# Performance work log

Hardware: AMD Instinct MI355X
Metric: run time of the kernel (lower is better)

## Reference

```python
import jax, jax.numpy as jnp
import numpy as np

N, T, U, V = 8, 200, 50, 500
BLANK = 0
EPS = 1e-10


def setup_inputs() -> dict:
    key = jax.random.key(0)
    k1, k2, k3, k4, k5 = jax.random.split(key, 5)
    logits = jax.random.normal(k1, (N, T, U, V), jnp.float32)
    teacher_logits = jax.random.normal(k2, (N, T, U, V), jnp.float32)
    y = jax.random.randint(k3, (N, U), 1, V)            # padded labels (blank=0 used as pad)
    x_lens = jax.random.randint(k4, (N,), T // 2, T + 1)  # valid encoder frames
    y_lens = jax.random.randint(k5, (N,), U // 2, U + 1)  # valid label lengths
    return {"logits": logits, "teacher_logits": teacher_logits, "y": y,
            "x_lens": x_lens, "y_lens": y_lens}


def reference(logits, teacher_logits, y, x_lens, y_lens):
    # Efficient RNNT-KD: collapse V-dim softmax into 3 classes (label, blank, rest).
    n, t, u, v = logits.shape
    s = jax.nn.softmax(logits, axis=-1)             # (N,T,U,V)
    te = jax.nn.softmax(teacher_logits, axis=-1)    # (N,T,U,V)

    idx = jnp.broadcast_to(y[:, None, :, None], (n, t, u, 1))  # label index per (n,t,u)
    py = jnp.take_along_axis(s, idx, axis=-1)       # (N,T,U,1)
    t_py = jnp.take_along_axis(te, idx, axis=-1)
    blank = s[..., BLANK:BLANK + 1]
    t_blank = te[..., BLANK:BLANK + 1]

    rem = 1.0 - py - blank
    t_rem = 1.0 - t_py - t_blank
    t_rem = jnp.where(t_rem < 0, EPS, t_rem)        # floor negative remainders (in-place set in torch)

    student = jnp.log(jnp.clip(jnp.concatenate([py, blank, rem], axis=-1), EPS, 1.0))  # (N,T,U,3)
    teacher = jnp.concatenate([t_py, t_blank, t_rem], axis=-1)                          # (N,T,U,3)

    t_mask = (jnp.arange(t)[None, :] < x_lens[:, None]).astype(student.dtype)[:, :, None, None]
    u_mask = (jnp.arange(u)[None, :] < y_lens[:, None]).astype(student.dtype)[:, None, :, None]
    m = t_mask * u_mask
    return jnp.stack([student * m, teacher * m])    # (2,N,T,U,3)
```

## Files before the change

kernel.cpp:

```cpp
#include <hip/hip_runtime.h>

#define N_ 8
#define T_ 200
#define U_ 50
#define V_ 500
#define NTU (N_ * T_ * U_)
#define EPSF 1e-10f

#define ROWS 16
#define ROWF (ROWS * V_)
#define FULLC 31

__global__ __launch_bounds__(256) void tkd_kernel(
    const float* __restrict__ lg,
    const float* __restrict__ tl,
    const int* __restrict__ y,
    const int* __restrict__ xlen,
    const int* __restrict__ ylen,
    float* __restrict__ out)
{
    __shared__ float bufA[ROWF];
    __shared__ float bufB[ROWF];

    const int tid  = threadIdx.x;
    const int wv   = tid >> 6;
    const int ln   = tid & 63;
    const int row0 = blockIdx.x * ROWS;

    const float* gA = lg + (size_t)row0 * V_;
    const float* gB = tl + (size_t)row0 * V_;

#pragma unroll
    for (int c = wv; c < FULLC; c += 4) {
        __builtin_amdgcn_global_load_lds(
            (const __attribute__((address_space(1))) void*)(gA + c * 256 + ln * 4),
            (__attribute__((address_space(3))) void*)(&bufA[c * 256 + ln * 4]),
            16, 0, 0);
    }
    if (wv == 3) {
        __builtin_amdgcn_global_load_lds(
            (const __attribute__((address_space(1))) void*)(gA + 7936 + ln),
            (__attribute__((address_space(3))) void*)(&bufA[7936 + ln]),
            4, 0, 0);
    }
#pragma unroll
    for (int c = wv; c < FULLC; c += 4) {
        __builtin_amdgcn_global_load_lds(
            (const __attribute__((address_space(1))) void*)(gB + c * 256 + ln * 4),
            (__attribute__((address_space(3))) void*)(&bufB[c * 256 + ln * 4]),
            16, 0, 0);
    }
    if (wv == 3) {
        __builtin_amdgcn_global_load_lds(
            (const __attribute__((address_space(1))) void*)(gB + 7936 + ln),
            (__attribute__((address_space(3))) void*)(&bufB[7936 + ln]),
            4, 0, 0);
    }

    const int g   = tid >> 4;
    const int l   = tid & 15;
    const int row = row0 + g;
    const int n   = row / (T_ * U_);
    const int r2  = row - n * (T_ * U_);
    const int t   = r2 / U_;
    const int u   = r2 - t * U_;
    const int yv  = y[n * U_ + u];
    const int xl  = xlen[n];
    const int yl  = ylen[n];

    asm volatile("s_waitcnt vmcnt(8)" ::: "memory");
    __builtin_amdgcn_s_barrier();
    asm volatile("" ::: "memory");

    const float* ra = &bufA[g * V_];
    const int   ltail = (l <= 12) ? l : 12;
    const float wmask = (l <= 12) ? 1.0f : 0.0f;
    float sA = 0.f;
#pragma unroll
    for (int j = 0; j < 7; ++j) {
        const float4 v = *reinterpret_cast<const float4*>(ra + (j * 16 + l) * 4);
        sA += __expf(v.x) + __expf(v.y) + __expf(v.z) + __expf(v.w);
    }
    {
        const float4 v = *reinterpret_cast<const float4*>(ra + (112 + ltail) * 4);
        sA += wmask * (__expf(v.x) + __expf(v.y) + __expf(v.z) + __expf(v.w));
    }
#pragma unroll
    for (int off = 1; off < 16; off <<= 1) sA += __shfl_xor(sA, off, 64);
    const float ay = ra[yv];
    const float a0 = ra[0];

    asm volatile("s_waitcnt vmcnt(0)" ::: "memory");
    __builtin_amdgcn_s_barrier();
    asm volatile("" ::: "memory");

    const float* rb = &bufB[g * V_];
    float sB = 0.f;
#pragma unroll
    for (int j = 0; j < 7; ++j) {
        const float4 v = *reinterpret_cast<const float4*>(rb + (j * 16 + l) * 4);
        sB += __expf(v.x) + __expf(v.y) + __expf(v.z) + __expf(v.w);
    }
    {
        const float4 v = *reinterpret_cast<const float4*>(rb + (112 + ltail) * 4);
        sB += wmask * (__expf(v.x) + __expf(v.y) + __expf(v.z) + __expf(v.w));
    }
#pragma unroll
    for (int off = 1; off < 16; off <<= 1) sB += __shfl_xor(sB, off, 64);
    const float by = rb[yv];
    const float b0 = rb[0];

    if (l == 0) {
        const float invA = 1.0f / sA;
        const float invB = 1.0f / sB;
        const float py   = __expf(ay) * invA;
        const float pbl  = __expf(a0) * invA;
        const float prem = 1.0f - py - pbl;
        const float tpy  = __expf(by) * invB;
        const float tbl  = __expf(b0) * invB;
        float trem = 1.0f - tpy - tbl;
        if (trem < 0.0f) trem = EPSF;

        const float s0 = __logf(fminf(fmaxf(py,   EPSF), 1.0f));
        const float s1 = __logf(fminf(fmaxf(pbl,  EPSF), 1.0f));
        const float s2 = __logf(fminf(fmaxf(prem, EPSF), 1.0f));

        const float mm = ((t < xl) && (u < yl)) ? 1.0f : 0.0f;

        const size_t o = (size_t)row * 3;
        out[o + 0] = s0 * mm;
        out[o + 1] = s1 * mm;
        out[o + 2] = s2 * mm;
        const size_t o2 = (size_t)NTU * 3 + o;
        out[o2 + 0] = tpy  * mm;
        out[o2 + 1] = tbl  * mm;
        out[o2 + 2] = trem * mm;
    }
}

extern "C" void kernel_launch(void* const* d_in, const int* in_sizes, int n_in,
                              void* d_out, int out_size, void* d_ws, size_t ws_size,
                              hipStream_t stream) {
    const float* lg = (const float*)d_in[0];
    const float* tl = (const float*)d_in[1];
    const int* y    = (const int*)d_in[2];
    const int* xlen = (const int*)d_in[3];
    const int* ylen = (const int*)d_in[4];
    float* out = (float*)d_out;

    tkd_kernel<<<NTU / ROWS, 256, 0, stream>>>(lg, tl, y, xlen, ylen, out);
}
```

Measured before the change: 324.4 us.

## Load teacher logits directly into registers, keep student via LDS DMA

Result: no change. 327.3 us (+0.9%).

```diff
diff --git a/kernel.cpp b/kernel.cpp
--- a/kernel.cpp
+++ b/kernel.cpp
@@ -20,16 +20,37 @@
     float* __restrict__ out)
 {
     __shared__ float bufA[ROWF];
-    __shared__ float bufB[ROWF];
 
     const int tid  = threadIdx.x;
     const int wv   = tid >> 6;
     const int ln   = tid & 63;
     const int row0 = blockIdx.x * ROWS;
 
+    const int g   = tid >> 4;
+    const int l   = tid & 15;
+    const int row = row0 + g;
+    const int n   = row / (T_ * U_);
+    const int r2  = row - n * (T_ * U_);
+    const int t   = r2 / U_;
+    const int u   = r2 - t * U_;
+    const int yv  = y[n * U_ + u];
+
+    const size_t base = (size_t)row * V_;
+    const float4* pb  = reinterpret_cast<const float4*>(tl + base);
+    const int ltail   = (l <= 12) ? l : 12;
+    float4 B0 = pb[0 * 16 + l];
+    float4 B1 = pb[1 * 16 + l];
+    float4 B2 = pb[2 * 16 + l];
+    float4 B3 = pb[3 * 16 + l];
+    float4 B4 = pb[4 * 16 + l];
+    float4 B5 = pb[5 * 16 + l];
+    float4 B6 = pb[6 * 16 + l];
+    float4 B7 = pb[112 + ltail];
+
+    const float by = tl[base + yv];
+    const float b0 = tl[base];
+
     const float* gA = lg + (size_t)row0 * V_;
-    const float* gB = tl + (size_t)row0 * V_;
-
 #pragma unroll
     for (int c = wv; c < FULLC; c += 4) {
         __builtin_amdgcn_global_load_lds(
@@ -43,38 +64,42 @@
             (__attribute__((address_space(3))) void*)(&bufA[7936 + ln]),
             4, 0, 0);
     }
+
+    float b00 = B0.x, b01 = B0.y, b02 = B0.z, b03 = B0.w;
+    float b04 = B1.x, b05 = B1.y, b06 = B1.z, b07 = B1.w;
+    float b08 = B2.x, b09 = B2.y, b10 = B2.z, b11 = B2.w;
+    float b12 = B3.x, b13 = B3.y, b14 = B3.z, b15 = B3.w;
+    float b16 = B4.x, b17 = B4.y, b18 = B4.z, b19 = B4.w;
+    float b20 = B5.x, b21 = B5.y, b22 = B5.z, b23 = B5.w;
+    float b24 = B6.x, b25 = B6.y, b26 = B6.z, b27 = B6.w;
+    float b28 = B7.x, b29 = B7.y, b30 = B7.z, b31 = B7.w;
+    asm volatile("" : "+v"(b00), "+v"(b01), "+v"(b02), "+v"(b03),
+                      "+v"(b04), "+v"(b05), "+v"(b06), "+v"(b07));
+    asm volatile("" : "+v"(b08), "+v"(b09), "+v"(b10), "+v"(b11),
+                      "+v"(b12), "+v"(b13), "+v"(b14), "+v"(b15));
+    asm volatile("" : "+v"(b16), "+v"(b17), "+v"(b18), "+v"(b19),
+                      "+v"(b20), "+v"(b21), "+v"(b22), "+v"(b23));
+    asm volatile("" : "+v"(b24), "+v"(b25), "+v"(b26), "+v"(b27),
+                      "+v"(b28), "+v"(b29), "+v"(b30), "+v"(b31));
+
+    const float wmask = (l <= 12) ? 1.0f : 0.0f;
+    float sB = 0.f;
+    sB += __expf(b00) + __expf(b01) + __expf(b02) + __expf(b03);
+    sB += __expf(b04) + __expf(b05) + __expf(b06) + __expf(b07);
+    sB += __expf(b08) + __expf(b09) + __expf(b10) + __expf(b11);
+    sB += __expf(b12) + __expf(b13) + __expf(b14) + __expf(b15);
+    sB += __expf(b16) + __expf(b17) + __expf(b18) + __expf(b19);
+    sB += __expf(b20) + __expf(b21) + __expf(b22) + __expf(b23);
+    sB += __expf(b24) + __expf(b25) + __expf(b26) + __expf(b27);
+    sB += wmask * (__expf(b28) + __expf(b29) + __expf(b30) + __expf(b31));
 #pragma unroll
-    for (int c = wv; c < FULLC; c += 4) {
-        __builtin_amdgcn_global_load_lds(
-            (const __attribute__((address_space(1))) void*)(gB + c * 256 + ln * 4),
-            (__attribute__((address_space(3))) void*)(&bufB[c * 256 + ln * 4]),
-            16, 0, 0);
-    }
-    if (wv == 3) {
-        __builtin_amdgcn_global_load_lds(
-            (const __attribute__((address_space(1))) void*)(gB + 7936 + ln),
-            (__attribute__((address_space(3))) void*)(&bufB[7936 + ln]),
-            4, 0, 0);
-    }
+    for (int off = 1; off < 16; off <<= 1) sB += __shfl_xor(sB, off, 64);
 
-    const int g   = tid >> 4;
-    const int l   = tid & 15;
-    const int row = row0 + g;
-    const int n   = row / (T_ * U_);
-    const int r2  = row - n * (T_ * U_);
-    const int t   = r2 / U_;
-    const int u   = r2 - t * U_;
-    const int yv  = y[n * U_ + u];
-    const int xl  = xlen[n];
-    const int yl  = ylen[n];
-
-    asm volatile("s_waitcnt vmcnt(8)" ::: "memory");
+    asm volatile("s_waitcnt vmcnt(0)" ::: "memory");
     __builtin_amdgcn_s_barrier();
     asm volatile("" ::: "memory");
 
     const float* ra = &bufA[g * V_];
-    const int   ltail = (l <= 12) ? l : 12;
-    const float wmask = (l <= 12) ? 1.0f : 0.0f;
     float sA = 0.f;
 #pragma unroll
     for (int j = 0; j < 7; ++j) {
@@ -89,26 +114,6 @@
     for (int off = 1; off < 16; off <<= 1) sA += __shfl_xor(sA, off, 64);
     const float ay = ra[yv];
     const float a0 = ra[0];
-
-    asm volatile("s_waitcnt vmcnt(0)" ::: "memory");
-    __builtin_amdgcn_s_barrier();
-    asm volatile("" ::: "memory");
-
-    const float* rb = &bufB[g * V_];
-    float sB = 0.f;
-#pragma unroll
-    for (int j = 0; j < 7; ++j) {
-        const float4 v = *reinterpret_cast<const float4*>(rb + (j * 16 + l) * 4);
-        sB += __expf(v.x) + __expf(v.y) + __expf(v.z) + __expf(v.w);
-    }
-    {
-        const float4 v = *reinterpret_cast<const float4*>(rb + (112 + ltail) * 4);
-        sB += wmask * (__expf(v.x) + __expf(v.y) + __expf(v.z) + __expf(v.w));
-    }
-#pragma unroll
-    for (int off = 1; off < 16; off <<= 1) sB += __shfl_xor(sB, off, 64);
-    const float by = rb[yv];
-    const float b0 = rb[0];
 
     if (l == 0) {
         const float invA = 1.0f / sA;
@@ -125,7 +130,7 @@
         const float s1 = __logf(fminf(fmaxf(pbl,  EPSF), 1.0f));
         const float s2 = __logf(fminf(fmaxf(prem, EPSF), 1.0f));
 
-        const float mm = ((t < xl) && (u < yl)) ? 1.0f : 0.0f;
+        const float mm = ((t < xlen[n]) && (u < ylen[n])) ? 1.0f : 0.0f;
 
         const size_t o = (size_t)row * 3;
         out[o + 0] = s0 * mm;
```
